# Kernel optimization log

Measured on AMD Instinct MI355X. Metric: run time of the kernel, lower is better.

The kernel has to match this reference:

```python
import jax, jax.numpy as jnp
import numpy as np

N = 50000
HEADS1, HIM = 8, 16
NEG_SLOPE = 0.2


def gat_conv(x, src, dst, W, a_src, a_dst, bias, heads, out_dim, concat):
    n = x.shape[0]
    h = (x @ W).reshape(n, heads, out_dim)                      # [N,H,D]
    al_src = jnp.einsum('nhd,hd->nh', h, a_src)                  # [N,H]
    al_dst = jnp.einsum('nhd,hd->nh', h, a_dst)                  # [N,H]
    e = jax.nn.leaky_relu(al_src[src] + al_dst[dst], NEG_SLOPE)  # [E,H]
    # segment softmax over incoming edges of each destination node
    e_max = jax.ops.segment_max(e, dst, num_segments=n)
    e_max = jnp.where(jnp.isfinite(e_max), e_max, 0.0)
    ex = jnp.exp(e - e_max[dst])
    denom = jax.ops.segment_sum(ex, dst, num_segments=n)
    denom = jnp.where(denom == 0.0, 1.0, denom)
    alpha = ex / denom[dst]                                      # [E,H]
    msg = h[src] * alpha[:, :, None]                             # [E,H,D]
    out = jax.ops.segment_sum(msg, dst, num_segments=n)          # [N,H,D]
    out = out.reshape(n, heads * out_dim) if concat else out.mean(axis=1)
    return out + bias


def setup_inputs() -> dict:
    key = jax.random.key(0)
    ks = jax.random.split(key, 12)
    num_feature, out_feature, him = 128, 121, HIM
    E = 800000
    x = jax.random.normal(ks[0], (N, num_feature), dtype=jnp.float32)
    edge_index = jax.random.randint(ks[1], (2, E), 0, N, dtype=jnp.int64)
    s = 0.1
    W1 = jax.random.normal(ks[2], (num_feature, HEADS1 * him), dtype=jnp.float32) * s
    a_src1 = jax.random.normal(ks[3], (HEADS1, him), dtype=jnp.float32) * s
    a_dst1 = jax.random.normal(ks[4], (HEADS1, him), dtype=jnp.float32) * s
    b1 = jnp.zeros((HEADS1 * him,), dtype=jnp.float32)
    W2 = jax.random.normal(ks[5], (HEADS1 * him, out_feature), dtype=jnp.float32) * s
    a_src2 = jax.random.normal(ks[6], (1, out_feature), dtype=jnp.float32) * s
    a_dst2 = jax.random.normal(ks[7], (1, out_feature), dtype=jnp.float32) * s
    b2 = jnp.zeros((out_feature,), dtype=jnp.float32)
    return {"x": x, "edge_index": edge_index, "W1": W1, "a_src1": a_src1,
            "a_dst1": a_dst1, "b1": b1, "W2": W2, "a_src2": a_src2,
            "a_dst2": a_dst2, "b2": b2}


def reference(x, edge_index, W1, a_src1, a_dst1, b1, W2, a_src2, a_dst2, b2):
    n = x.shape[0]
    loops = jnp.arange(n, dtype=edge_index.dtype)
    src = jnp.concatenate([edge_index[0], loops])  # add self-loops (PyG default)
    dst = jnp.concatenate([edge_index[1], loops])
    h = gat_conv(x, src, dst, W1, a_src1, a_dst1, b1, HEADS1, HIM, True)
    h = jax.nn.relu(h)
    out = gat_conv(h, src, dst, W2, a_src2, a_dst2, b2, 1, W2.shape[1], True)
    return out
```

## Files before the change

kernel.cpp:

```cpp
#include <hip/hip_runtime.h>
#include <hip/hip_fp16.h>

#define NEG_SLOPE 0.2f

typedef __fp16 half8v __attribute__((ext_vector_type(8)));
typedef __fp16 half4v __attribute__((ext_vector_type(4)));
typedef float f32x4 __attribute__((ext_vector_type(4)));
typedef unsigned uint4u __attribute__((ext_vector_type(4), aligned(4)));
typedef float f32x4u __attribute__((ext_vector_type(4), aligned(4)));

__device__ __forceinline__ float lrelu(float x) {
    return fmaxf(x, 0.0f) + NEG_SLOPE * fminf(x, 0.0f);
}

__device__ __forceinline__ unsigned fkey(float f) {
    unsigned u = __float_as_uint(f);
    return (u & 0x80000000u) ? ~u : (u | 0x80000000u);
}
__device__ __forceinline__ float funkey(unsigned k) {
    return __uint_as_float((k & 0x80000000u) ? (k & 0x7fffffffu) : ~k);
}


__global__ __launch_bounds__(256) void scan_reduce(const int* __restrict__ cnt,
                                                   int* __restrict__ bsum, int n) {
    __shared__ int sm[256];
    int base = blockIdx.x * 1024 + threadIdx.x * 4;
    int s = 0;
#pragma unroll
    for (int j = 0; j < 4; ++j) {
        int i = base + j;
        if (i < n) s += cnt[i];
    }
    sm[threadIdx.x] = s;
    __syncthreads();
#pragma unroll
    for (int off = 128; off >= 1; off >>= 1) {
        if (threadIdx.x < off) sm[threadIdx.x] += sm[threadIdx.x + off];
        __syncthreads();
    }
    if (threadIdx.x == 0) bsum[blockIdx.x] = sm[0];
}

__global__ __launch_bounds__(256) void scan_write2(const int* __restrict__ cnt,
                                                   const int* __restrict__ bsum,
                                                   int* __restrict__ rp, int n) {
    __shared__ int sm[256];
    __shared__ int boff;
    int tid = threadIdx.x;
    int partial = (tid < blockIdx.x) ? bsum[tid] : 0;
    sm[tid] = partial;
    __syncthreads();
#pragma unroll
    for (int off = 128; off >= 1; off >>= 1) {
        if (tid < off) sm[tid] += sm[tid + off];
        __syncthreads();
    }
    if (tid == 0) boff = sm[0];
    __syncthreads();

    int base = blockIdx.x * 1024 + tid * 4;
    int v[4];
    int s = 0;
#pragma unroll
    for (int j = 0; j < 4; ++j) {
        int i = base + j;
        v[j] = (i < n) ? cnt[i] : 0;
        s += v[j];
    }
    sm[tid] = s;
    __syncthreads();
#pragma unroll
    for (int off = 1; off < 256; off <<= 1) {
        int y = (tid >= off) ? sm[tid - off] : 0;
        __syncthreads();
        sm[tid] += y;
        __syncthreads();
    }
    int run = sm[tid] - s + boff;
#pragma unroll
    for (int j = 0; j < 4; ++j) {
        int i = base + j;
        if (i < n) {
            rp[i] = run;
            run += v[j];
            if (i == n - 1) rp[n] = run;
        }
    }
}


__global__ __launch_bounds__(256) void rhist1_kernel(const int* __restrict__ dst,
                                                     int* __restrict__ h, int E, int nblk) {
    __shared__ int lh[256];
    lh[threadIdx.x] = 0;
    __syncthreads();
    int base = blockIdx.x * 1024;
#pragma unroll
    for (int j = 0; j < 4; ++j) {
        int i = base + j * 256 + threadIdx.x;
        if (i < E) atomicAdd(&lh[dst[i] & 255], 1);
    }
    __syncthreads();
    h[threadIdx.x * nblk + blockIdx.x] = lh[threadIdx.x];
}

__global__ __launch_bounds__(256) void rhist2_kernel(const unsigned* __restrict__ kv,
                                                     int* __restrict__ h, int E, int nblk) {
    __shared__ int lh[256];
    lh[threadIdx.x] = 0;
    __syncthreads();
    int base = blockIdx.x * 1024;
#pragma unroll
    for (int j = 0; j < 4; ++j) {
        int i = base + j * 256 + threadIdx.x;
        if (i < E) atomicAdd(&lh[kv[i] >> 24], 1);
    }
    __syncthreads();
    h[threadIdx.x * nblk + blockIdx.x] = lh[threadIdx.x];
}

template <int SH, bool PACK>
__global__ __launch_bounds__(256) void rscat_kernel(const unsigned* __restrict__ in,
                                                    const int* __restrict__ srcp,
                                                    const int* __restrict__ dstp,
                                                    unsigned* __restrict__ outv,
                                                    const int* __restrict__ scanned,
                                                    int E, int nblk) {
    __shared__ unsigned items[1024];
    __shared__ unsigned sorted[1024];
    __shared__ int lh[256], lstart[256], rbase[256];
    __shared__ int wcnt[4][256];

    int tid = threadIdx.x, blk = blockIdx.x;
    int base = blk * 1024;
    int k = min(1024, E - base);
    lh[tid] = 0;
    rbase[tid] = 0;
#pragma unroll
    for (int j = 0; j < 4; ++j) {
        int idx = j * 256 + tid;
        unsigned v = 0u;
        if (base + idx < E) {
            if constexpr (PACK)
                v = ((unsigned)dstp[base + idx] << 16) | (unsigned)srcp[base + idx];
            else
                v = in[base + idx];
        }
        items[idx] = v;
    }
    __syncthreads();
#pragma unroll
    for (int j = 0; j < 4; ++j) {
        int idx = j * 256 + tid;
        if (idx < k) atomicAdd(&lh[(items[idx] >> SH) & 255], 1);
    }
    __syncthreads();
    int sv = lh[tid];
    lstart[tid] = sv;
    __syncthreads();
    for (int off = 1; off < 256; off <<= 1) {
        int y = (tid >= off) ? lstart[tid - off] : 0;
        __syncthreads();
        lstart[tid] += y;
        __syncthreads();
    }
    int excl = lstart[tid] - sv;
    __syncthreads();
    lstart[tid] = excl;
    __syncthreads();

    int lane = tid & 63, wave = tid >> 6;
#pragma unroll
    for (int it = 0; it < 4; ++it) {
        int idx = it * 256 + tid;
        unsigned v = items[idx];
        int d = (v >> SH) & 255;
        bool valid = idx < k;
        unsigned long long m = __ballot(valid);
#pragma unroll
        for (int b = 0; b < 8; ++b) {
            unsigned long long bb = __ballot((d >> b) & 1);
            m &= ((d >> b) & 1) ? bb : ~bb;
        }
        int lanerank = __popcll(m & ((1ull << lane) - 1ull));
        int wtot = __popcll(m);
        wcnt[0][tid] = 0; wcnt[1][tid] = 0; wcnt[2][tid] = 0; wcnt[3][tid] = 0;
        __syncthreads();
        if (valid && lanerank == 0) wcnt[wave][d] = wtot;
        __syncthreads();
        if (valid) {
            int cw = 0;
            for (int w = 0; w < wave; ++w) cw += wcnt[w][d];
            sorted[lstart[d] + rbase[d] + cw + lanerank] = v;
        }
        __syncthreads();
        rbase[tid] += wcnt[0][tid] + wcnt[1][tid] + wcnt[2][tid] + wcnt[3][tid];
        __syncthreads();
    }
#pragma unroll
    for (int j = 0; j < 4; ++j) {
        int i = j * 256 + tid;
        if (i < k) {
            unsigned v = sorted[i];
            int d = (v >> SH) & 255;
            outv[scanned[d * nblk + blk] + (i - lstart[d])] = v;
        }
    }
}


__global__ void rp_kernel(const unsigned* __restrict__ kv, int* __restrict__ rp,
                          int E, int N) {
    int i = blockIdx.x * 256 + threadIdx.x;
    if (i >= E) return;
    int cur = (int)(kv[i] >> 16);
    int prev = (i == 0) ? -1 : (int)(kv[i - 1] >> 16);
    for (int t = prev + 1; t <= cur; ++t) rp[t] = i;
    if (i == E - 1)
        for (int t = cur + 1; t <= N; ++t) rp[t] = E;
}


template <int H>
__global__ __launch_bounds__(256) void gmax_kernel(const float* __restrict__ a,
                                                   unsigned* __restrict__ gm, int total) {
    __shared__ unsigned sm[256];
    unsigned loc = 0;
    int stride = 256 * gridDim.x;
    for (int i = blockIdx.x * 256 + threadIdx.x; i < total; i += stride)
        loc = max(loc, fkey(a[i]));
    sm[threadIdx.x] = loc;
    __syncthreads();
    for (int off = 128; off >= H; off >>= 1) {
        if (threadIdx.x < off) sm[threadIdx.x] = max(sm[threadIdx.x], sm[threadIdx.x + off]);
        __syncthreads();
    }
    if (threadIdx.x < H) atomicMax(&gm[threadIdx.x], sm[threadIdx.x]);
}


__global__ __launch_bounds__(256) void w1_kernel(const unsigned* __restrict__ kv,
                                                 const float* __restrict__ alS,
                                                 const float* __restrict__ alD,
                                                 const unsigned* __restrict__ gm,
                                                 __half* __restrict__ w1t, int E) {
    int e = blockIdx.x * 256 + threadIdx.x;
    if (e >= E) return;
    unsigned k = kv[e];
    int s = (int)(k & 0xFFFFu), t = (int)(k >> 16);
    float sv[8], dv[8];
    *(f32x4*)&sv[0] = *(const f32x4*)(alS + (size_t)s * 8);
    *(f32x4*)&sv[4] = *(const f32x4*)(alS + (size_t)s * 8 + 4);
    *(f32x4*)&dv[0] = *(const f32x4*)(alD + (size_t)t * 8);
    *(f32x4*)&dv[4] = *(const f32x4*)(alD + (size_t)t * 8 + 4);
#pragma unroll
    for (int h = 0; h < 8; ++h) {
        float m = lrelu(funkey(gm[h]) + dv[h]);
        w1t[(size_t)h * E + e] = __float2half(__expf(lrelu(sv[h] + dv[h]) - m));
    }
}

__global__ void w2_kernel(const unsigned* __restrict__ kv, const float* __restrict__ alS,
                          const float* __restrict__ alD, const unsigned* __restrict__ gm,
                          float* __restrict__ w2v, int E) {
    int e = blockIdx.x * 256 + threadIdx.x;
    if (e >= E) return;
    unsigned k = kv[e];
    int s = (int)(k & 0xFFFFu), t = (int)(k >> 16);
    float adT = alD[t];
    w2v[e] = __expf(lrelu(alS[s] + adT) - lrelu(funkey(gm[0]) + adT));
}


template <int NC, typename AT, bool FUSE_AL2>
__global__ __launch_bounds__(256) void gemm_mfma(const AT* __restrict__ A,
                                                 const float* __restrict__ B,
                                                 __half* __restrict__ C, int M,
                                                 const float* __restrict__ as,
                                                 const float* __restrict__ ad,
                                                 float* __restrict__ alS,
                                                 float* __restrict__ alD) {
    __shared__ __half Bt[128][136];

    {
        int t = threadIdx.x;
        int c = t & 127;
        int kq = t >> 7;
#pragma unroll
        for (int ch = 0; ch < 8; ++ch) {
            int k0 = kq * 64 + ch * 8;
            half8v hv;
#pragma unroll
            for (int j = 0; j < 8; ++j) {
                float v = (c < NC) ? B[(size_t)(k0 + j) * NC + c] : 0.0f;
                hv[j] = (__fp16)v;
            }
            *(half8v*)&Bt[c][k0] = hv;
        }
    }
    __syncthreads();

    const int wid = threadIdx.x >> 6;
    const int lane = threadIdx.x & 63;
    const int li = lane & 15;
    const int lg = lane >> 4;

    int row = blockIdx.x * 64 + wid * 16 + li;
    int rowc = min(row, M - 1);

    half8v a[4];
#pragma unroll
    for (int ks = 0; ks < 4; ++ks) {
        int q = ks * 4 + lg;
        if constexpr (sizeof(AT) == 2) {
            a[ks] = *((const half8v*)(A + (size_t)rowc * 128) + q);
        } else {
            const float4* p = (const float4*)(A + (size_t)rowc * 128) + 2 * q;
            float4 a0 = p[0], a1 = p[1];
            half8v hv;
            hv[0] = (__fp16)a0.x; hv[1] = (__fp16)a0.y; hv[2] = (__fp16)a0.z; hv[3] = (__fp16)a0.w;
            hv[4] = (__fp16)a1.x; hv[5] = (__fp16)a1.y; hv[6] = (__fp16)a1.z; hv[7] = (__fp16)a1.w;
            a[ks] = hv;
        }
    }

    f32x4 acc[8];
#pragma unroll
    for (int ct = 0; ct < 8; ++ct) acc[ct] = (f32x4)0.0f;

#pragma unroll
    for (int ks = 0; ks < 4; ++ks) {
#pragma unroll
        for (int ct = 0; ct < 8; ++ct) {
            half8v b = *(const half8v*)&Bt[ct * 16 + li][ks * 32 + 8 * lg];
            acc[ct] = __builtin_amdgcn_mfma_f32_16x16x32_f16(a[ks], b, acc[ct], 0, 0, 0);
        }
    }

    int orow = blockIdx.x * 64 + wid * 16 + 4 * lg;
#pragma unroll
    for (int ct = 0; ct < 8; ++ct) {
#pragma unroll
        for (int r = 0; r < 4; ++r) {
            int rr = orow + r;
            if (rr < M) C[(size_t)rr * 128 + ct * 16 + li] = __float2half(acc[ct][r]);
        }
    }

    if constexpr (FUSE_AL2) {
        float asv[8], adv[8];
#pragma unroll
        for (int ct = 0; ct < 8; ++ct) {
            int c = ct * 16 + li;
            asv[ct] = (c < NC) ? as[c] : 0.0f;
            adv[ct] = (c < NC) ? ad[c] : 0.0f;
        }
#pragma unroll
        for (int r = 0; r < 4; ++r) {
            float s = 0.f, d = 0.f;
#pragma unroll
            for (int ct = 0; ct < 8; ++ct) {
                s = fmaf(acc[ct][r], asv[ct], s);
                d = fmaf(acc[ct][r], adv[ct], d);
            }
            s += __shfl_down(s, 8); d += __shfl_down(d, 8);
            s += __shfl_down(s, 4); d += __shfl_down(d, 4);
            s += __shfl_down(s, 2); d += __shfl_down(d, 2);
            s += __shfl_down(s, 1); d += __shfl_down(d, 1);
            if (li == 0) {
                int rr = orow + r;
                if (rr < M) { alS[rr] = s; alD[rr] = d; }
            }
        }
    }
}


__global__ void al1_kernel(const __half* __restrict__ h1h, const float* __restrict__ as,
                           const float* __restrict__ ad, float* __restrict__ alS,
                           float* __restrict__ alD, int N) {
    int g = blockIdx.x * 256 + threadIdx.x;
    if (g >= N * 8) return;
    int r = g >> 3, h = g & 7;
    const __half2* hp = (const __half2*)(h1h + (size_t)r * 128 + h * 16);
    const float* sp = as + h * 16;
    const float* dp = ad + h * 16;
    float s = 0.f, d = 0.f;
#pragma unroll
    for (int q = 0; q < 8; ++q) {
        float2 v = __half22float2(hp[q]);
        s = fmaf(v.x, sp[2 * q], s);
        d = fmaf(v.x, dp[2 * q], d);
        s = fmaf(v.y, sp[2 * q + 1], s);
        d = fmaf(v.y, dp[2 * q + 1], d);
    }
    alS[g] = s;
    alD[g] = d;
}


__global__ __launch_bounds__(256) void agg1_kernel(
    const __half* __restrict__ h1h, const float* __restrict__ alS,
    const float* __restrict__ alD, const float* __restrict__ b1,
    const int* __restrict__ rp, const unsigned* __restrict__ kv,
    const __half* __restrict__ w1t, const unsigned* __restrict__ gm,
    __half* __restrict__ h2h, int N, int E) {
    int t = blockIdx.x * 4 + (threadIdx.x >> 6);
    int lane = threadIdx.x & 63;
    int h = lane >> 3;

    float adh = alD[t * 8 + h];
    float mh = lrelu(funkey(gm[h]) + adh);
    int e0 = rp[t], e1 = rp[t + 1];

    float ex = __expf(lrelu(alS[t * 8 + h] + adh) - mh);
    float dsum = ex, dsum2 = 0.f;
    float2 hs = __half22float2(*(const __half2*)(h1h + (size_t)t * 128 + 2 * lane));
    float fx = ex * hs.x, fy = ex * hs.y;
    const __half* wrow = w1t + (size_t)h * E;

    int e = e0;
    while (e < e1 && (e & 3)) {
        int s0 = (int)(kv[e] & 0xFFFFu);
        float w0 = __half2float(wrow[e]);
        float2 f0 = __half22float2(*(const __half2*)(h1h + (size_t)s0 * 128 + 2 * lane));
        dsum2 += w0;
        fx = fmaf(w0, f0.x, fx); fy = fmaf(w0, f0.y, fy);
        ++e;
    }
    for (; e + 16 <= e1; e += 16) {
        uint4u kk[4];
        float ww[16];
#pragma unroll
        for (int q = 0; q < 4; ++q) {
            kk[q] = *(const uint4u*)&kv[e + 4 * q];
            half4v wv = *(const half4v*)&wrow[e + 4 * q];
#pragma unroll
            for (int r = 0; r < 4; ++r) ww[q * 4 + r] = (float)wv[r];
        }
        float2 ff[16];
#pragma unroll
        for (int q = 0; q < 4; ++q)
#pragma unroll
            for (int r = 0; r < 4; ++r)
                ff[q * 4 + r] = __half22float2(
                    *(const __half2*)(h1h + (size_t)(kk[q][r] & 0xFFFFu) * 128 + 2 * lane));
#pragma unroll
        for (int q = 0; q < 4; ++q) {
            if (q & 1) dsum2 += (ww[q * 4] + ww[q * 4 + 1]) + (ww[q * 4 + 2] + ww[q * 4 + 3]);
            else       dsum  += (ww[q * 4] + ww[q * 4 + 1]) + (ww[q * 4 + 2] + ww[q * 4 + 3]);
#pragma unroll
            for (int r = 0; r < 4; ++r) {
                float w = ww[q * 4 + r];
                float2 f = ff[q * 4 + r];
                fx = fmaf(w, f.x, fx);
                fy = fmaf(w, f.y, fy);
            }
        }
    }
    if (e + 8 <= e1) {
        uint4u ka = *(const uint4u*)&kv[e];
        uint4u kb = *(const uint4u*)&kv[e + 4];
        half4v wva = *(const half4v*)&wrow[e];
        half4v wvb = *(const half4v*)&wrow[e + 4];
        float2 f0 = __half22float2(*(const __half2*)(h1h + (size_t)(ka.x & 0xFFFFu) * 128 + 2 * lane));
        float2 f1 = __half22float2(*(const __half2*)(h1h + (size_t)(ka.y & 0xFFFFu) * 128 + 2 * lane));
        float2 f2 = __half22float2(*(const __half2*)(h1h + (size_t)(ka.z & 0xFFFFu) * 128 + 2 * lane));
        float2 f3 = __half22float2(*(const __half2*)(h1h + (size_t)(ka.w & 0xFFFFu) * 128 + 2 * lane));
        float2 f4 = __half22float2(*(const __half2*)(h1h + (size_t)(kb.x & 0xFFFFu) * 128 + 2 * lane));
        float2 f5 = __half22float2(*(const __half2*)(h1h + (size_t)(kb.y & 0xFFFFu) * 128 + 2 * lane));
        float2 f6 = __half22float2(*(const __half2*)(h1h + (size_t)(kb.z & 0xFFFFu) * 128 + 2 * lane));
        float2 f7 = __half22float2(*(const __half2*)(h1h + (size_t)(kb.w & 0xFFFFu) * 128 + 2 * lane));
        float w0 = (float)wva[0], w1 = (float)wva[1], w2 = (float)wva[2], w3 = (float)wva[3];
        float w4 = (float)wvb[0], w5 = (float)wvb[1], w6 = (float)wvb[2], w7 = (float)wvb[3];
        dsum += (w0 + w1) + (w2 + w3);
        dsum2 += (w4 + w5) + (w6 + w7);
        fx = fmaf(w0, f0.x, fx); fy = fmaf(w0, f0.y, fy);
        fx = fmaf(w1, f1.x, fx); fy = fmaf(w1, f1.y, fy);
        fx = fmaf(w2, f2.x, fx); fy = fmaf(w2, f2.y, fy);
        fx = fmaf(w3, f3.x, fx); fy = fmaf(w3, f3.y, fy);
        fx = fmaf(w4, f4.x, fx); fy = fmaf(w4, f4.y, fy);
        fx = fmaf(w5, f5.x, fx); fy = fmaf(w5, f5.y, fy);
        fx = fmaf(w6, f6.x, fx); fy = fmaf(w6, f6.y, fy);
        fx = fmaf(w7, f7.x, fx); fy = fmaf(w7, f7.y, fy);
        e += 8;
    }
    if (e + 4 <= e1) {
        uint4u ka = *(const uint4u*)&kv[e];
        half4v wva = *(const half4v*)&wrow[e];
        float2 f0 = __half22float2(*(const __half2*)(h1h + (size_t)(ka.x & 0xFFFFu) * 128 + 2 * lane));
        float2 f1 = __half22float2(*(const __half2*)(h1h + (size_t)(ka.y & 0xFFFFu) * 128 + 2 * lane));
        float2 f2 = __half22float2(*(const __half2*)(h1h + (size_t)(ka.z & 0xFFFFu) * 128 + 2 * lane));
        float2 f3 = __half22float2(*(const __half2*)(h1h + (size_t)(ka.w & 0xFFFFu) * 128 + 2 * lane));
        float w0 = (float)wva[0], w1 = (float)wva[1], w2 = (float)wva[2], w3 = (float)wva[3];
        dsum += (w0 + w1) + (w2 + w3);
        fx = fmaf(w0, f0.x, fx); fy = fmaf(w0, f0.y, fy);
        fx = fmaf(w1, f1.x, fx); fy = fmaf(w1, f1.y, fy);
        fx = fmaf(w2, f2.x, fx); fy = fmaf(w2, f2.y, fy);
        fx = fmaf(w3, f3.x, fx); fy = fmaf(w3, f3.y, fy);
        e += 4;
    }
    for (; e < e1; ++e) {
        int s0 = (int)(kv[e] & 0xFFFFu);
        float w0 = __half2float(wrow[e]);
        float2 f0 = __half22float2(*(const __half2*)(h1h + (size_t)s0 * 128 + 2 * lane));
        dsum2 += w0;
        fx = fmaf(w0, f0.x, fx); fy = fmaf(w0, f0.y, fy);
    }
    dsum += dsum2;
    float inv = 1.0f / dsum;
    float2 bb = *(const float2*)(b1 + 2 * lane);
    float ox = fmaxf(fmaf(fx, inv, bb.x), 0.0f);
    float oy = fmaxf(fmaf(fy, inv, bb.y), 0.0f);
    *(__half2*)(h2h + (size_t)t * 128 + 2 * lane) = __floats2half2_rn(ox, oy);
}


__global__ __launch_bounds__(256) void agg2_kernel(
    const __half* __restrict__ h3h, const float* __restrict__ alS,
    const float* __restrict__ alD, const float* __restrict__ b2,
    const int* __restrict__ rp, const unsigned* __restrict__ kv,
    const float* __restrict__ w2v, const unsigned* __restrict__ gm,
    float* __restrict__ out, int N, int NC) {
    int t = blockIdx.x * 4 + (threadIdx.x >> 6);
    int lane = threadIdx.x & 63;

    float adT = alD[t];
    float m = lrelu(funkey(gm[0]) + adT);
    int e0 = rp[t], e1 = rp[t + 1];

    float ex = __expf(lrelu(alS[t] + adT) - m);
    float dsum = ex, dsum2 = 0.f;
    float2 hs = __half22float2(*(const __half2*)(h3h + (size_t)t * 128 + 2 * lane));
    float fx = ex * hs.x, fy = ex * hs.y;

    int e = e0;
    for (; e + 16 <= e1; e += 16) {
        uint4u kk[4];
        f32x4u ww[4];
#pragma unroll
        for (int q = 0; q < 4; ++q) {
            kk[q] = *(const uint4u*)&kv[e + 4 * q];
            ww[q] = *(const f32x4u*)&w2v[e + 4 * q];
        }
        float2 ff[16];
#pragma unroll
        for (int q = 0; q < 4; ++q)
#pragma unroll
            for (int r = 0; r < 4; ++r)
                ff[q * 4 + r] = __half22float2(
                    *(const __half2*)(h3h + (size_t)(kk[q][r] & 0xFFFFu) * 128 + 2 * lane));
#pragma unroll
        for (int q = 0; q < 4; ++q) {
            if (q & 1) dsum2 += (ww[q][0] + ww[q][1]) + (ww[q][2] + ww[q][3]);
            else       dsum  += (ww[q][0] + ww[q][1]) + (ww[q][2] + ww[q][3]);
#pragma unroll
            for (int r = 0; r < 4; ++r) {
                float w = ww[q][r];
                float2 f = ff[q * 4 + r];
                fx = fmaf(w, f.x, fx);
                fy = fmaf(w, f.y, fy);
            }
        }
    }
    if (e + 8 <= e1) {
        uint4u ka = *(const uint4u*)&kv[e];
        uint4u kb = *(const uint4u*)&kv[e + 4];
        f32x4u wa = *(const f32x4u*)&w2v[e];
        f32x4u wb = *(const f32x4u*)&w2v[e + 4];
        float2 f0 = __half22float2(*(const __half2*)(h3h + (size_t)(ka.x & 0xFFFFu) * 128 + 2 * lane));
        float2 f1 = __half22float2(*(const __half2*)(h3h + (size_t)(ka.y & 0xFFFFu) * 128 + 2 * lane));
        float2 f2 = __half22float2(*(const __half2*)(h3h + (size_t)(ka.z & 0xFFFFu) * 128 + 2 * lane));
        float2 f3 = __half22float2(*(const __half2*)(h3h + (size_t)(ka.w & 0xFFFFu) * 128 + 2 * lane));
        float2 f4 = __half22float2(*(const __half2*)(h3h + (size_t)(kb.x & 0xFFFFu) * 128 + 2 * lane));
        float2 f5 = __half22float2(*(const __half2*)(h3h + (size_t)(kb.y & 0xFFFFu) * 128 + 2 * lane));
        float2 f6 = __half22float2(*(const __half2*)(h3h + (size_t)(kb.z & 0xFFFFu) * 128 + 2 * lane));
        float2 f7 = __half22float2(*(const __half2*)(h3h + (size_t)(kb.w & 0xFFFFu) * 128 + 2 * lane));
        dsum += (wa[0] + wa[1]) + (wa[2] + wa[3]);
        dsum2 += (wb[0] + wb[1]) + (wb[2] + wb[3]);
        fx = fmaf(wa[0], f0.x, fx); fy = fmaf(wa[0], f0.y, fy);
        fx = fmaf(wa[1], f1.x, fx); fy = fmaf(wa[1], f1.y, fy);
        fx = fmaf(wa[2], f2.x, fx); fy = fmaf(wa[2], f2.y, fy);
        fx = fmaf(wa[3], f3.x, fx); fy = fmaf(wa[3], f3.y, fy);
        fx = fmaf(wb[0], f4.x, fx); fy = fmaf(wb[0], f4.y, fy);
        fx = fmaf(wb[1], f5.x, fx); fy = fmaf(wb[1], f5.y, fy);
        fx = fmaf(wb[2], f6.x, fx); fy = fmaf(wb[2], f6.y, fy);
        fx = fmaf(wb[3], f7.x, fx); fy = fmaf(wb[3], f7.y, fy);
        e += 8;
    }
    if (e + 4 <= e1) {
        uint4u ka = *(const uint4u*)&kv[e];
        f32x4u wa = *(const f32x4u*)&w2v[e];
        float2 f0 = __half22float2(*(const __half2*)(h3h + (size_t)(ka.x & 0xFFFFu) * 128 + 2 * lane));
        float2 f1 = __half22float2(*(const __half2*)(h3h + (size_t)(ka.y & 0xFFFFu) * 128 + 2 * lane));
        float2 f2 = __half22float2(*(const __half2*)(h3h + (size_t)(ka.z & 0xFFFFu) * 128 + 2 * lane));
        float2 f3 = __half22float2(*(const __half2*)(h3h + (size_t)(ka.w & 0xFFFFu) * 128 + 2 * lane));
        dsum += (wa[0] + wa[1]) + (wa[2] + wa[3]);
        fx = fmaf(wa[0], f0.x, fx); fy = fmaf(wa[0], f0.y, fy);
        fx = fmaf(wa[1], f1.x, fx); fy = fmaf(wa[1], f1.y, fy);
        fx = fmaf(wa[2], f2.x, fx); fy = fmaf(wa[2], f2.y, fy);
        fx = fmaf(wa[3], f3.x, fx); fy = fmaf(wa[3], f3.y, fy);
        e += 4;
    }
    for (; e < e1; ++e) {
        int s0 = (int)(kv[e] & 0xFFFFu);
        float w0 = w2v[e];
        float2 f0 = __half22float2(*(const __half2*)(h3h + (size_t)s0 * 128 + 2 * lane));
        dsum2 += w0;
        fx = fmaf(w0, f0.x, fx); fy = fmaf(w0, f0.y, fy);
    }
    dsum += dsum2;
    float inv = 1.0f / dsum;
    int c0 = 2 * lane, c1 = 2 * lane + 1;
    if (c0 < NC) out[(size_t)t * NC + c0] = fmaf(fx, inv, b2[c0]);
    if (c1 < NC) out[(size_t)t * NC + c1] = fmaf(fy, inv, b2[c1]);
}


extern "C" void kernel_launch(void* const* d_in, const int* in_sizes, int n_in,
                              void* d_out, int out_size, void* d_ws, size_t ws_size,
                              hipStream_t stream) {
    const float* x   = (const float*)d_in[0];
    const int*   ei  = (const int*)d_in[1];
    const float* W1  = (const float*)d_in[2];
    const float* aS1 = (const float*)d_in[3];
    const float* aD1 = (const float*)d_in[4];
    const float* b1  = (const float*)d_in[5];
    const float* W2  = (const float*)d_in[6];
    const float* aS2 = (const float*)d_in[7];
    const float* aD2 = (const float*)d_in[8];
    const float* b2  = (const float*)d_in[9];
    float* out = (float*)d_out;

    const int N = in_sizes[0] / 128;
    const int E = in_sizes[1] / 2;
    const int NC2 = 121;

    const int NBLK = (E + 1023) / 1024;
    const int HN = 256 * NBLK;

    size_t off = 0;
    auto alloc = [&](size_t bytes) {
        size_t o = off;
        off = (off + bytes + 255) & ~(size_t)255;
        return o;
    };
    char* ws = (char*)d_ws;
    unsigned* kv0  = (unsigned*)(ws + alloc((size_t)E * 4));
    unsigned* kv1  = (unsigned*)(ws + alloc((size_t)E * 4));
    int*      h    = (int*)(ws + alloc((size_t)(HN + 1) * 4));
    int*      hs   = (int*)(ws + alloc((size_t)(HN + 1) * 4));
    int*      bsum = (int*)(ws + alloc(256 * 4));
    int*      rp   = (int*)(ws + alloc((size_t)(N + 1) * 4));
    float*    alS1 = (float*)(ws + alloc((size_t)N * 8 * 4));
    float*    alD1 = (float*)(ws + alloc((size_t)N * 8 * 4));
    float*    alS2 = (float*)(ws + alloc((size_t)N * 4));
    float*    alD2 = (float*)(ws + alloc((size_t)N * 4));
    unsigned* gm1  = (unsigned*)(ws + alloc(8 * 4));
    unsigned* gm2  = (unsigned*)(ws + alloc(4));
    __half*   w1t  = (__half*)(ws + alloc((size_t)E * 8 * 2));
    __half*   h1h  = (__half*)(ws + alloc((size_t)N * 128 * 2));
    __half*   h2h  = (__half*)(ws + alloc((size_t)N * 128 * 2));
    __half*   h3h  = h1h;
    float*    w2v  = (float*)kv1;
    if (ws_size < off) return;

    const int* src = ei;
    const int* dst = ei + E;

    hipMemsetAsync(gm1, 0, 8 * 4, stream);
    hipMemsetAsync(gm2, 0, 4, stream);

    int eb = (E + 255) / 256;
    int snb = (HN + 1023) / 1024;

    rhist1_kernel<<<NBLK, 256, 0, stream>>>(dst, h, E, NBLK);
    scan_reduce<<<snb, 256, 0, stream>>>(h, bsum, HN);
    scan_write2<<<snb, 256, 0, stream>>>(h, bsum, hs, HN);
    rscat_kernel<16, true><<<NBLK, 256, 0, stream>>>(nullptr, src, dst, kv1, hs, E, NBLK);
    rhist2_kernel<<<NBLK, 256, 0, stream>>>(kv1, h, E, NBLK);
    scan_reduce<<<snb, 256, 0, stream>>>(h, bsum, HN);
    scan_write2<<<snb, 256, 0, stream>>>(h, bsum, hs, HN);
    rscat_kernel<24, false><<<NBLK, 256, 0, stream>>>(kv1, nullptr, nullptr, kv0, hs, E, NBLK);
    rp_kernel<<<eb, 256, 0, stream>>>(kv0, rp, E, N);

    int gmb = (N + 63) / 64;
    int ab = (N + 3) / 4;
    gemm_mfma<128, float, false><<<gmb, 256, 0, stream>>>(x, W1, h1h, N,
                                                          nullptr, nullptr, nullptr, nullptr);
    al1_kernel<<<(N * 8 + 255) / 256, 256, 0, stream>>>(h1h, aS1, aD1, alS1, alD1, N);
    gmax_kernel<8><<<128, 256, 0, stream>>>(alS1, gm1, N * 8);
    w1_kernel<<<eb, 256, 0, stream>>>(kv0, alS1, alD1, gm1, w1t, E);
    agg1_kernel<<<ab, 256, 0, stream>>>(h1h, alS1, alD1, b1, rp, kv0, w1t, gm1, h2h, N, E);

    gemm_mfma<121, __half, true><<<gmb, 256, 0, stream>>>(h2h, W2, h3h, N,
                                                          aS2, aD2, alS2, alD2);
    gmax_kernel<1><<<128, 256, 0, stream>>>(alS2, gm2, N);
    w2_kernel<<<eb, 256, 0, stream>>>(kv0, alS2, alD2, gm2, w2v, E);
    agg2_kernel<<<ab, 256, 0, stream>>>(h3h, alS2, alD2, b2, rp, kv0, w2v, gm2, out, N, NC2);
}
```

Baseline: 198.3 us.

## Add a third radix pass so edges are also sorted by source within each destination

The edge radix sort previously ran two passes keyed on dst bits only. It now runs three passes on a packed key whose low byte comes from src bits, so edges are ordered by source within each destination segment. The intent is more coherent gathers of h[src] and alpha in the aggregation kernels. The cost is an extra histogram, scan and scatter pass over all edges. The sort key layout also changes, so it must stay consistent with the packing done inside rscat_kernel.

```diff
diff --git a/kernel.cpp b/kernel.cpp
--- a/kernel.cpp
+++ b/kernel.cpp
@@ -90,8 +90,8 @@
 }
 
 
-__global__ __launch_bounds__(256) void rhist1_kernel(const int* __restrict__ dst,
-                                                     int* __restrict__ h, int E, int nblk) {
+__global__ __launch_bounds__(256) void rhist_pack(const int* __restrict__ srcp,
+                                                  int* __restrict__ h, int E, int nblk) {
     __shared__ int lh[256];
     lh[threadIdx.x] = 0;
     __syncthreads();
@@ -99,14 +99,15 @@
 #pragma unroll
     for (int j = 0; j < 4; ++j) {
         int i = base + j * 256 + threadIdx.x;
-        if (i < E) atomicAdd(&lh[dst[i] & 255], 1);
+        if (i < E) atomicAdd(&lh[(srcp[i] >> 8) & 255], 1);
     }
     __syncthreads();
     h[threadIdx.x * nblk + blockIdx.x] = lh[threadIdx.x];
 }
 
-__global__ __launch_bounds__(256) void rhist2_kernel(const unsigned* __restrict__ kv,
-                                                     int* __restrict__ h, int E, int nblk) {
+template <int SH>
+__global__ __launch_bounds__(256) void rhist_kv(const unsigned* __restrict__ kv,
+                                                int* __restrict__ h, int E, int nblk) {
     __shared__ int lh[256];
     lh[threadIdx.x] = 0;
     __syncthreads();
@@ -114,7 +115,7 @@
 #pragma unroll
     for (int j = 0; j < 4; ++j) {
         int i = base + j * 256 + threadIdx.x;
-        if (i < E) atomicAdd(&lh[kv[i] >> 24], 1);
+        if (i < E) atomicAdd(&lh[(kv[i] >> SH) & 255], 1);
     }
     __syncthreads();
     h[threadIdx.x * nblk + blockIdx.x] = lh[threadIdx.x];
@@ -647,8 +648,8 @@
         return o;
     };
     char* ws = (char*)d_ws;
-    unsigned* kv0  = (unsigned*)(ws + alloc((size_t)E * 4));
-    unsigned* kv1  = (unsigned*)(ws + alloc((size_t)E * 4));
+    unsigned* kvA  = (unsigned*)(ws + alloc((size_t)E * 4));
+    unsigned* kvB  = (unsigned*)(ws + alloc((size_t)E * 4));
     int*      h    = (int*)(ws + alloc((size_t)(HN + 1) * 4));
     int*      hs   = (int*)(ws + alloc((size_t)(HN + 1) * 4));
     int*      bsum = (int*)(ws + alloc(256 * 4));
@@ -663,7 +664,7 @@
     __half*   h1h  = (__half*)(ws + alloc((size_t)N * 128 * 2));
     __half*   h2h  = (__half*)(ws + alloc((size_t)N * 128 * 2));
     __half*   h3h  = h1h;
-    float*    w2v  = (float*)kv1;
+    float*    w2v  = (float*)kvB;
     if (ws_size < off) return;
 
     const int* src = ei;
@@ -675,15 +676,22 @@
     int eb = (E + 255) / 256;
     int snb = (HN + 1023) / 1024;
 
-    rhist1_kernel<<<NBLK, 256, 0, stream>>>(dst, h, E, NBLK);
+    rhist_pack<<<NBLK, 256, 0, stream>>>(src, h, E, NBLK);
     scan_reduce<<<snb, 256, 0, stream>>>(h, bsum, HN);
     scan_write2<<<snb, 256, 0, stream>>>(h, bsum, hs, HN);
-    rscat_kernel<16, true><<<NBLK, 256, 0, stream>>>(nullptr, src, dst, kv1, hs, E, NBLK);
-    rhist2_kernel<<<NBLK, 256, 0, stream>>>(kv1, h, E, NBLK);
+    rscat_kernel<8, true><<<NBLK, 256, 0, stream>>>(nullptr, src, dst, kvA, hs, E, NBLK);
+
+    rhist_kv<16><<<NBLK, 256, 0, stream>>>(kvA, h, E, NBLK);
     scan_reduce<<<snb, 256, 0, stream>>>(h, bsum, HN);
     scan_write2<<<snb, 256, 0, stream>>>(h, bsum, hs, HN);
-    rscat_kernel<24, false><<<NBLK, 256, 0, stream>>>(kv1, nullptr, nullptr, kv0, hs, E, NBLK);
-    rp_kernel<<<eb, 256, 0, stream>>>(kv0, rp, E, N);
+    rscat_kernel<16, false><<<NBLK, 256, 0, stream>>>(kvA, nullptr, nullptr, kvB, hs, E, NBLK);
+
+    rhist_kv<24><<<NBLK, 256, 0, stream>>>(kvB, h, E, NBLK);
+    scan_reduce<<<snb, 256, 0, stream>>>(h, bsum, HN);
+    scan_write2<<<snb, 256, 0, stream>>>(h, bsum, hs, HN);
+    rscat_kernel<24, false><<<NBLK, 256, 0, stream>>>(kvB, nullptr, nullptr, kvA, hs, E, NBLK);
+
+    rp_kernel<<<eb, 256, 0, stream>>>(kvA, rp, E, N);
 
     int gmb = (N + 63) / 64;
     int ab = (N + 3) / 4;
@@ -691,12 +699,12 @@
                                                           nullptr, nullptr, nullptr, nullptr);
     al1_kernel<<<(N * 8 + 255) / 256, 256, 0, stream>>>(h1h, aS1, aD1, alS1, alD1, N);
     gmax_kernel<8><<<128, 256, 0, stream>>>(alS1, gm1, N * 8);
-    w1_kernel<<<eb, 256, 0, stream>>>(kv0, alS1, alD1, gm1, w1t, E);
-    agg1_kernel<<<ab, 256, 0, stream>>>(h1h, alS1, alD1, b1, rp, kv0, w1t, gm1, h2h, N, E);
+    w1_kernel<<<eb, 256, 0, stream>>>(kvA, alS1, alD1, gm1, w1t, E);
+    agg1_kernel<<<ab, 256, 0, stream>>>(h1h, alS1, alD1, b1, rp, kvA, w1t, gm1, h2h, N, E);
 
     gemm_mfma<121, __half, true><<<gmb, 256, 0, stream>>>(h2h, W2, h3h, N,
                                                           aS2, aD2, alS2, alD2);
     gmax_kernel<1><<<128, 256, 0, stream>>>(alS2, gm2, N);
-    w2_kernel<<<eb, 256, 0, stream>>>(kv0, alS2, alD2, gm2, w2v, E);
-    agg2_kernel<<<ab, 256, 0, stream>>>(h3h, alS2, alD2, b2, rp, kv0, w2v, gm2, out, N, NC2);
-}
+    w2_kernel<<<eb, 256, 0, stream>>>(kvA, alS2, alD2, gm2, w2v, E);
+    agg2_kernel<<<ab, 256, 0, stream>>>(h3h, alS2, alD2, b2, rp, kvA, w2v, gm2, out, N, NC2);
+}
```

New measurement: 219.9 us. +10.9%, slower.
